# Performance work log

Measured on AMD Instinct MI355X. Metric: run time of the kernel, lower is better.

Reference implementation:

```python
import jax, jax.numpy as jnp
import numpy as np
from jax import lax

L = 2048        # leaves per tree
VOCAB = 50000
IN_DIM = 300
MEM = 150
HID = 50
NCLS = 5


def _balanced_tree(n_leaf):
    # children-before-parent topological order; node ids: [0, n_leaf) leaves,
    # [n_leaf, 2*n_leaf-1) internal, last id is the root's single child (ROOT is passthrough).
    level = list(range(n_leaf)); nid = n_leaf; lefts = []; rights = []
    while len(level) > 1:
        nxt = []
        for j in range(0, len(level) - 1, 2):
            lefts.append(level[j]); rights.append(level[j + 1]); nxt.append(nid); nid += 1
        if len(level) % 2:
            nxt.append(level[-1])
        level = nxt
    return np.asarray(lefts, np.int32), np.asarray(rights, np.int32)


def setup_inputs() -> dict:
    key = jax.random.key(0)
    ks = jax.random.split(key, 12)
    left, right = _balanced_tree(L)
    s = 0.05
    return {
        "l_tokens": jax.random.randint(ks[0], (L,), 0, VOCAB, dtype=jnp.int32),
        "r_tokens": jax.random.randint(ks[1], (L,), 0, VOCAB, dtype=jnp.int32),
        "left_idx": jnp.asarray(left),
        "right_idx": jnp.asarray(right),
        "emb": jax.random.normal(ks[2], (VOCAB, IN_DIM), jnp.float32) * s,
        "W_ioux": jax.random.normal(ks[3], (IN_DIM, 3 * MEM), jnp.float32) * s,
        "b_ioux": jnp.zeros((3 * MEM,), jnp.float32),
        "W_iouh": jax.random.normal(ks[4], (MEM, 3 * MEM), jnp.float32) * s,
        "b_iouh": jnp.zeros((3 * MEM,), jnp.float32),
        "W_fx": jax.random.normal(ks[5], (IN_DIM, MEM), jnp.float32) * s,
        "b_fx": jnp.zeros((MEM,), jnp.float32),
        "W_fh": jax.random.normal(ks[6], (MEM, MEM), jnp.float32) * s,
        "b_fh": jnp.zeros((MEM,), jnp.float32),
        "W_attn": jax.random.normal(ks[7], (2 * MEM, MEM), jnp.float32) * s,
        "b_attn": jnp.zeros((MEM,), jnp.float32),
        "W_wh": jax.random.normal(ks[8], (2 * MEM, HID), jnp.float32) * s,
        "b_wh": jnp.zeros((HID,), jnp.float32),
        "W_wp": jax.random.normal(ks[9], (HID, NCLS), jnp.float32) * s,
        "b_wp": jnp.zeros((NCLS,), jnp.float32),
    }


def _gates(iou):
    i, o, u = jnp.split(iou, 3, axis=-1)
    return jax.nn.sigmoid(i), jax.nn.sigmoid(o), jnp.tanh(u)


def _tree_lstm(tokens, left, right, emb, W_ioux, b_ioux, W_iouh, b_iouh, W_fh, b_fh):
    # Leaves (child_c = child_h = 0): iou = ioux(x) + iouh(0); fc term vanishes.
    x = emb[tokens]                                   # [L, in_dim]
    i, o, u = _gates(x @ W_ioux + b_ioux + b_iouh)
    c_leaf = i * u
    h_leaf = o * jnp.tanh(c_leaf)
    n_leaf = tokens.shape[0]
    N = 2 * n_leaf - 1
    C = jnp.zeros((N, MEM), x.dtype).at[:n_leaf].set(c_leaf)
    H = jnp.zeros((N, MEM), x.dtype).at[:n_leaf].set(h_leaf)

    # Internal nodes (inputs=None branch): iou = iouh(sum h_child); f_k = sigmoid(fh(h_k)).
    def step(carry, inp):
        C, H = carry
        k, li, ri = inp
        hl, hr = H[li], H[ri]
        i, o, u = _gates((hl + hr) @ W_iouh + b_iouh)
        fl = jax.nn.sigmoid(hl @ W_fh + b_fh)
        fr = jax.nn.sigmoid(hr @ W_fh + b_fh)
        c = i * u + fl * C[li] + fr * C[ri]
        h = o * jnp.tanh(c)
        return (C.at[k].set(c), H.at[k].set(h)), None

    ids = jnp.arange(n_leaf, N, dtype=jnp.int32)
    (C, H), _ = lax.scan(step, (C, H), (ids, left, right))
    return H  # [N, MEM]; H[-1] is the root hidden state (ROOT is passthrough)


def reference(l_tokens, r_tokens, left_idx, right_idx, emb, W_ioux, b_ioux, W_iouh, b_iouh, W_fx, b_fx, W_fh, b_fh, W_attn, b_attn, W_wh, b_wh, W_wp, b_wp):
    Hl = _tree_lstm(l_tokens, left_idx, right_idx, emb, W_ioux, b_ioux, W_iouh, b_iouh, W_fh, b_fh)
    Hr = _tree_lstm(r_tokens, left_idx, right_idx, emb, W_ioux, b_ioux, W_iouh, b_iouh, W_fh, b_fh)
    # Soft cross-attention over all node hidden states (torch code builds [Nr,Nl,m] beta;
    # here expressed as matmuls -- identical math).
    scores = Hl @ Hr.T                               # [Nl, Nr]
    beta_sum = jax.nn.softmax(scores, axis=1) @ Hr    # [Nl, MEM]
    alpha_sum = jax.nn.softmax(scores.T, axis=1) @ Hl  # [Nr, MEM]
    v_l = jnp.concatenate([Hl, beta_sum], axis=1) @ W_attn + b_attn
    v_r = jnp.concatenate([Hr, alpha_sum], axis=1) @ W_attn + b_attn
    lh = v_l[-1:]  # root hidden (root_idx is the root's matched row)
    rh = v_r[-1:]
    feats = jnp.concatenate([lh * rh, jnp.abs(lh - rh)], axis=1)
    hid = jax.nn.sigmoid(feats @ W_wh + b_wh)
    return jax.nn.log_softmax(hid @ W_wp + b_wp, axis=-1)  # [1, NCLS]
```

## Files before the change

kernel.cpp:

```cpp
#include <hip/hip_runtime.h>
#include <math.h>

#define LEAVES 2048
#define NN     4095
#define MEMD   150
#define IOUD   450
#define IND    300
#define STR    152
#define CT     4096


__device__ __forceinline__ float sigf(float x) { return 1.f / (1.f + expf(-x)); }

__global__ __launch_bounds__(256) void k_pack(
    const float* __restrict__ Wx, const float* __restrict__ Wh,
    const float* __restrict__ Wf,
    float4* __restrict__ PWx, float4* __restrict__ PWhf)
{
    int i = blockIdx.x * 256 + threadIdx.x;
    if (i < 45000) {
        int k = i / 150, d = i - k * 150;
        float4 v;
        v.x = Wx[k * IOUD + d];
        v.y = Wx[k * IOUD + 150 + d];
        v.z = Wx[k * IOUD + 300 + d];
        v.w = 0.f;
        PWx[i] = v;
    } else if (i < 67500) {
        int j = i - 45000;
        int k = j / 150, d = j - k * 150;
        float4 v;
        v.x = Wh[k * IOUD + d];
        v.y = Wh[k * IOUD + 150 + d];
        v.z = Wh[k * IOUD + 300 + d];
        v.w = Wf[k * MEMD + d];
        PWhf[j] = v;
    }
}

__global__ __launch_bounds__(640) void k_leaf(
    const int* __restrict__ ltok, const int* __restrict__ rtok,
    const float* __restrict__ emb, const float4* __restrict__ PWx,
    const float* __restrict__ bx, const float* __restrict__ bh,
    float* __restrict__ C, float* __restrict__ H)
{
    __shared__ float xs[IND][8];
    __shared__ int   tok[8];
    __shared__ float pb[300][13];
    const int tree = blockIdx.y, t = threadIdx.x;
    const int leaf0 = blockIdx.x << 3;
    const int* toks = tree ? rtok : ltok;

    if (t < 8) tok[t] = toks[leaf0 + t];
    __syncthreads();
    if (t < 600) {
        int q = t >> 3, m = t & 7;
        float4 v = *(const float4*)(emb + (size_t)tok[m] * IND + 4 * q);
        xs[4*q+0][m] = v.x; xs[4*q+1][m] = v.y;
        xs[4*q+2][m] = v.z; xs[4*q+3][m] = v.w;
    }
    __syncthreads();

    const int kh = (t >= 320) ? 1 : 0;
    const int tt = t - 320 * kh;
    const bool act = (tt < 300);
    const int hf = (tt >= 150) ? 1 : 0;
    const int d  = tt - 150 * hf;
    const int m0 = hf * 4;

    float ai[4], ao[4], au[4];
    if (act) {
        if (kh == 0) {
            const float bi = bx[d]       + bh[d];
            const float bo = bx[d + 150] + bh[d + 150];
            const float bu = bx[d + 300] + bh[d + 300];
            #pragma unroll
            for (int m = 0; m < 4; ++m) { ai[m] = bi; ao[m] = bo; au[m] = bu; }
        } else {
            #pragma unroll
            for (int m = 0; m < 4; ++m) { ai[m] = 0.f; ao[m] = 0.f; au[m] = 0.f; }
        }
        const float4* wp = PWx + d;
        const int kb = kh * 150;
        #pragma unroll 5
        for (int kk = 0; kk < 150; ++kk) {
            const int k = kb + kk;
            float4 w = wp[(size_t)k * 150];
            float4 x4 = *(const float4*)(&xs[k][m0]);
            float xv[4] = {x4.x, x4.y, x4.z, x4.w};
            #pragma unroll
            for (int m = 0; m < 4; ++m) {
                ai[m] = fmaf(xv[m], w.x, ai[m]);
                ao[m] = fmaf(xv[m], w.y, ao[m]);
                au[m] = fmaf(xv[m], w.z, au[m]);
            }
        }
    }
    if (kh == 1 && act) {
        #pragma unroll
        for (int m = 0; m < 4; ++m) {
            pb[tt][3*m + 0] = ai[m];
            pb[tt][3*m + 1] = ao[m];
            pb[tt][3*m + 2] = au[m];
        }
    }
    __syncthreads();
    if (kh == 0 && act) {
        float* Ct = C + ((size_t)tree * CT + leaf0 + m0) * STR;
        float* Ht = H + ((size_t)tree * CT + leaf0 + m0) * STR;
        #pragma unroll
        for (int m = 0; m < 4; ++m) {
            float aiv = ai[m] + pb[tt][3*m + 0];
            float aov = ao[m] + pb[tt][3*m + 1];
            float auv = au[m] + pb[tt][3*m + 2];
            float c = sigf(aiv) * tanhf(auv);
            float h = sigf(aov) * tanhf(c);
            Ct[(size_t)m * STR + d] = c;
            Ht[(size_t)m * STR + d] = h;
        }
    }
}

__global__ __launch_bounds__(640) void k_lvl(
    const float4* __restrict__ PWhf, const float* __restrict__ bh,
    const float* __restrict__ bf,
    float* __restrict__ C, float* __restrict__ H, int PB, int CB)
{
    __shared__ float buf[MEMD][8];
    __shared__ float pb[300][11];
    const int tree = blockIdx.y, t = threadIdx.x;
    const int p0 = blockIdx.x * 4;
    float* Ct = C + (size_t)tree * CT * STR;
    float* Ht = H + (size_t)tree * CT * STR;

    if (t < 600) {
        int m = t / 150, d2 = t - m * 150;
        int cc = CB + 2 * (p0 + m);
        float a = Ht[(size_t)cc * STR + d2];
        float b = Ht[(size_t)(cc + 1) * STR + d2];
        buf[d2][2*m + 0] = a + b;
        buf[d2][2*m + 1] = a;
    }
    __syncthreads();

    const int kh = (t >= 320) ? 1 : 0;
    const int tt = t - 320 * kh;
    const bool act = (tt < 300);
    const int hf = (tt >= 150) ? 1 : 0;
    const int d  = tt - 150 * hf;
    const int m0 = hf * 2;

    float ai[2], ao[2], au[2], afs[2], afl[2], cl[2], cr[2];
    if (act) {
        if (kh == 0) {
            const float bi = bh[d], bo = bh[d + 150], bu = bh[d + 300], bfv = bf[d];
            #pragma unroll
            for (int m = 0; m < 2; ++m) {
                ai[m] = bi; ao[m] = bo; au[m] = bu;
                afs[m] = 2.f * bfv; afl[m] = bfv;
                int cc = CB + 2 * (p0 + m0 + m);
                cl[m] = Ct[(size_t)cc * STR + d];
                cr[m] = Ct[(size_t)(cc + 1) * STR + d];
            }
        } else {
            #pragma unroll
            for (int m = 0; m < 2; ++m) {
                ai[m] = 0.f; ao[m] = 0.f; au[m] = 0.f; afs[m] = 0.f; afl[m] = 0.f;
            }
        }
        const float4* wp = PWhf + d;
        const int kb = kh * 75;
        #pragma unroll 5
        for (int kk = 0; kk < 75; ++kk) {
            const int k = kb + kk;
            float4 w = wp[(size_t)k * 150];
            float4 p4 = *(const float4*)(&buf[k][2 * m0]);
            float hs0 = p4.x, hl0 = p4.y, hs1 = p4.z, hl1 = p4.w;
            ai[0]  = fmaf(hs0, w.x, ai[0]);   ai[1]  = fmaf(hs1, w.x, ai[1]);
            ao[0]  = fmaf(hs0, w.y, ao[0]);   ao[1]  = fmaf(hs1, w.y, ao[1]);
            au[0]  = fmaf(hs0, w.z, au[0]);   au[1]  = fmaf(hs1, w.z, au[1]);
            afs[0] = fmaf(hs0, w.w, afs[0]);  afs[1] = fmaf(hs1, w.w, afs[1]);
            afl[0] = fmaf(hl0, w.w, afl[0]);  afl[1] = fmaf(hl1, w.w, afl[1]);
        }
    }
    if (kh == 1 && act) {
        #pragma unroll
        for (int m = 0; m < 2; ++m) {
            pb[tt][5*m + 0] = ai[m];
            pb[tt][5*m + 1] = ao[m];
            pb[tt][5*m + 2] = au[m];
            pb[tt][5*m + 3] = afs[m];
            pb[tt][5*m + 4] = afl[m];
        }
    }
    __syncthreads();
    if (kh == 0 && act) {
        #pragma unroll
        for (int m = 0; m < 2; ++m) {
            float aiv  = ai[m]  + pb[tt][5*m + 0];
            float aov  = ao[m]  + pb[tt][5*m + 1];
            float auv  = au[m]  + pb[tt][5*m + 2];
            float afsv = afs[m] + pb[tt][5*m + 3];
            float aflv = afl[m] + pb[tt][5*m + 4];
            float frv = afsv - aflv;
            float c = sigf(aiv) * tanhf(auv) + sigf(aflv) * cl[m] + sigf(frv) * cr[m];
            float h = sigf(aov) * tanhf(c);
            size_t rw = (size_t)(PB + p0 + m0 + m) * STR + d;
            Ct[rw] = c;
            Ht[rw] = h;
        }
    }
}

__global__ __launch_bounds__(640) void k_node(
    const float4* __restrict__ PWhf, const float* __restrict__ bh,
    const float* __restrict__ bf,
    float* __restrict__ C, float* __restrict__ H, int PB, int CB)
{
    __shared__ float hsv[MEMD], hlv[MEMD];
    __shared__ float part[4][5][152];
    const int tree = blockIdx.y, node = blockIdx.x, t = threadIdx.x;
    float* Ct = C + (size_t)tree * CT * STR;
    float* Ht = H + (size_t)tree * CT * STR;
    const int c0 = CB + 2 * node;

    if (t < MEMD) {
        float a = Ht[(size_t)c0 * STR + t];
        float b = Ht[(size_t)(c0 + 1) * STR + t];
        hsv[t] = a + b;
        hlv[t] = a;
    }
    __syncthreads();

    const int grp = t / 160, d = t - grp * 160;
    if (d < MEMD) {
        const int k0 = (grp * MEMD) >> 2;
        const int k1 = ((grp + 1) * MEMD) >> 2;
        float ai = 0.f, ao = 0.f, au = 0.f, afs = 0.f, afl = 0.f;
        const float4* wp = PWhf + d;
        #pragma unroll 4
        for (int k = k0; k < k1; ++k) {
            float4 w = wp[(size_t)k * 150];
            float hs = hsv[k], hl = hlv[k];
            ai  = fmaf(hs, w.x, ai);
            ao  = fmaf(hs, w.y, ao);
            au  = fmaf(hs, w.z, au);
            afs = fmaf(hs, w.w, afs);
            afl = fmaf(hl, w.w, afl);
        }
        part[grp][0][d] = ai;  part[grp][1][d] = ao;  part[grp][2][d] = au;
        part[grp][3][d] = afs; part[grp][4][d] = afl;
    }
    __syncthreads();

    if (t < MEMD) {
        const int d2 = t;
        float ai = bh[d2], ao = bh[d2 + 150], au = bh[d2 + 300];
        float bfv = bf[d2];
        float afs = 2.f * bfv, afl = bfv;
        #pragma unroll
        for (int g = 0; g < 4; ++g) {
            ai  += part[g][0][d2]; ao  += part[g][1][d2]; au += part[g][2][d2];
            afs += part[g][3][d2]; afl += part[g][4][d2];
        }
        float cl = Ct[(size_t)c0 * STR + d2];
        float cr = Ct[(size_t)(c0 + 1) * STR + d2];
        float frv = afs - afl;
        float c = sigf(ai) * tanhf(au) + sigf(afl) * cl + sigf(frv) * cr;
        float h = sigf(ao) * tanhf(c);
        size_t rw = (size_t)(PB + node) * STR + d2;
        Ct[rw] = c;
        Ht[rw] = h;
    }
}

__global__ __launch_bounds__(256) void k_attn(
    const float* __restrict__ H, float* __restrict__ cstat, float* __restrict__ part)
{
    __shared__ float lv[MEMD];
    __shared__ float sc[64];
    __shared__ float pv[64];
    const int bid = blockIdx.x, t = threadIdx.x;
    const int side = bid >> 6, chunk = bid & 63;
    const int j0 = chunk << 6;
    const int jn = min(64, NN - j0);
    const float* lastrow = H + ((size_t)side * CT + (NN - 1)) * STR;
    if (t < MEMD) lv[t] = lastrow[t];
    __syncthreads();

    const float* src = H + (size_t)(side ^ 1) * CT * STR + (size_t)j0 * STR;
    const int wave = t >> 6, lane = t & 63;
    for (int r = wave; r < jn; r += 4) {
        const float* row = src + (size_t)r * STR;
        float a = lv[lane] * row[lane] + lv[lane + 64] * row[lane + 64];
        if (lane < 22) a += lv[lane + 128] * row[lane + 128];
        #pragma unroll
        for (int off = 32; off; off >>= 1) a += __shfl_xor(a, off);
        if (lane == 0) sc[r] = a;
    }
    __syncthreads();
    if (wave == 0) {
        float v = (lane < jn) ? sc[lane] : -3.4e38f;
        float m = v;
        #pragma unroll
        for (int off = 32; off; off >>= 1) m = fmaxf(m, __shfl_xor(m, off));
        float e = (lane < jn) ? expf(v - m) : 0.f;
        pv[lane] = e;
        float s = e;
        #pragma unroll
        for (int off = 32; off; off >>= 1) s += __shfl_xor(s, off);
        if (lane == 0) {
            cstat[(side * 64 + chunk) * 2 + 0] = m;
            cstat[(side * 64 + chunk) * 2 + 1] = s;
        }
    }
    __syncthreads();
    if (t < MEMD) {
        float a = 0.f;
        for (int j = 0; j < jn; ++j) a += pv[j] * src[(size_t)j * STR + t];
        part[(size_t)(side * 64 + chunk) * STR + t] = a;
    }
}

__global__ __launch_bounds__(512) void k_final(
    const float* __restrict__ H, const float* __restrict__ cstat,
    const float* __restrict__ part,
    const float* __restrict__ Wattn, const float* __restrict__ battn,
    const float* __restrict__ Wwh, const float* __restrict__ bwh,
    const float* __restrict__ Wwp, const float* __restrict__ bwp,
    float* __restrict__ outp)
{
    __shared__ float scl[2][64];
    __shared__ float gseS[2];
    __shared__ float ba[300], catl[300], catr[300], vl[150], vr[150];
    __shared__ float feats[300], hid[50], logits[5];
    const int t = threadIdx.x, wave = t >> 6, lane = t & 63;

    if (wave < 2) {
        float lm = cstat[(wave * 64 + lane) * 2 + 0];
        float ls = cstat[(wave * 64 + lane) * 2 + 1];
        float m = lm;
        #pragma unroll
        for (int off = 32; off; off >>= 1) m = fmaxf(m, __shfl_xor(m, off));
        float s = expf(lm - m);
        scl[wave][lane] = s;
        float se = ls * s;
        #pragma unroll
        for (int off = 32; off; off >>= 1) se += __shfl_xor(se, off);
        if (lane == 0) gseS[wave] = se;
    }
    __syncthreads();
    if (t < 300) {
        int side = t / MEMD, d = t - side * MEMD;
        float a = 0.f;
        for (int c = 0; c < 64; ++c)
            a += part[(size_t)(side * 64 + c) * STR + d] * scl[side][c];
        ba[t] = a / gseS[side];
    }
    __syncthreads();
    const float* Hl_last = H + (size_t)(0 * CT + NN - 1) * STR;
    const float* Hr_last = H + (size_t)(1 * CT + NN - 1) * STR;
    if (t < MEMD) {
        catl[t] = Hl_last[t]; catl[150 + t] = ba[t];
        catr[t] = Hr_last[t]; catr[150 + t] = ba[150 + t];
    }
    __syncthreads();
    if (t < 300) {
        int d = (t < 150) ? t : t - 150;
        const float* cat = (t < 150) ? catl : catr;
        float a = battn[d];
        for (int k = 0; k < 300; ++k) a = fmaf(cat[k], Wattn[k * 150 + d], a);
        if (t < 150) vl[d] = a; else vr[d] = a;
    }
    __syncthreads();
    if (t < MEMD) {
        feats[t] = vl[t] * vr[t];
        feats[150 + t] = fabsf(vl[t] - vr[t]);
    }
    __syncthreads();
    if (t < 50) {
        float a = bwh[t];
        for (int k = 0; k < 300; ++k) a = fmaf(feats[k], Wwh[k * 50 + t], a);
        hid[t] = sigf(a);
    }
    __syncthreads();
    if (t < 5) {
        float a = bwp[t];
        for (int g = 0; g < 50; ++g) a = fmaf(hid[g], Wwp[g * 5 + t], a);
        logits[t] = a;
    }
    __syncthreads();
    if (t == 0) {
        float m = logits[0];
        for (int c = 1; c < 5; ++c) m = fmaxf(m, logits[c]);
        float s = 0.f;
        for (int c = 0; c < 5; ++c) s += expf(logits[c] - m);
        float lse = m + logf(s);
        for (int c = 0; c < 5; ++c) outp[c] = logits[c] - lse;
    }
}

extern "C" void kernel_launch(void* const* d_in, const int* in_sizes, int n_in,
                              void* d_out, int out_size, void* d_ws, size_t ws_size,
                              hipStream_t stream)
{
    const int*   ltok  = (const int*)d_in[0];
    const int*   rtok  = (const int*)d_in[1];
    const float* emb   = (const float*)d_in[4];
    const float* Wx    = (const float*)d_in[5];
    const float* bx    = (const float*)d_in[6];
    const float* Wh    = (const float*)d_in[7];
    const float* bh    = (const float*)d_in[8];
    const float* Wf    = (const float*)d_in[11];
    const float* bf    = (const float*)d_in[12];
    const float* Wattn = (const float*)d_in[13];
    const float* battn = (const float*)d_in[14];
    const float* Wwh   = (const float*)d_in[15];
    const float* bwh   = (const float*)d_in[16];
    const float* Wwp   = (const float*)d_in[17];
    const float* bwp   = (const float*)d_in[18];
    float* out = (float*)d_out;

    float* ws    = (float*)d_ws;
    float*  C    = ws;
    float*  H    = C + (size_t)2 * CT * STR;
    float*  cs   = H + (size_t)2 * CT * STR;
    float*  part = cs + 256;
    float4* PWx  = (float4*)(part + (size_t)128 * STR);
    float4* PWhf = PWx + 45000;

    k_pack<<<dim3(264), dim3(256), 0, stream>>>(Wx, Wh, Wf, PWx, PWhf);

    k_leaf<<<dim3(256, 2), dim3(640), 0, stream>>>(ltok, rtok, emb, PWx, bx, bh, C, H);

    k_lvl<<<dim3(256, 2), dim3(640), 0, stream>>>(PWhf, bh, bf, C, H, 2048, 0);
    k_lvl<<<dim3(128, 2), dim3(640), 0, stream>>>(PWhf, bh, bf, C, H, 3072, 2048);
    k_lvl<<<dim3(64,  2), dim3(640), 0, stream>>>(PWhf, bh, bf, C, H, 3584, 3072);

    k_node<<<dim3(128, 2), dim3(640), 0, stream>>>(PWhf, bh, bf, C, H, 3840, 3584);
    k_node<<<dim3(64,  2), dim3(640), 0, stream>>>(PWhf, bh, bf, C, H, 3968, 3840);
    k_node<<<dim3(32,  2), dim3(640), 0, stream>>>(PWhf, bh, bf, C, H, 4032, 3968);
    k_node<<<dim3(16,  2), dim3(640), 0, stream>>>(PWhf, bh, bf, C, H, 4064, 4032);
    k_node<<<dim3(8,   2), dim3(640), 0, stream>>>(PWhf, bh, bf, C, H, 4080, 4064);
    k_node<<<dim3(4,   2), dim3(640), 0, stream>>>(PWhf, bh, bf, C, H, 4088, 4080);
    k_node<<<dim3(2,   2), dim3(640), 0, stream>>>(PWhf, bh, bf, C, H, 4092, 4088);
    k_node<<<dim3(1,   2), dim3(640), 0, stream>>>(PWhf, bh, bf, C, H, 4094, 4092);

    k_attn<<<dim3(128), dim3(256), 0, stream>>>(H, cs, part);
    k_final<<<dim3(1), dim3(512), 0, stream>>>(H, cs, part, Wattn, battn,
                                               Wwh, bwh, Wwp, bwp, out);
}
```

Baseline: 150.5 us.

## Drop Wx packing and restructure leaf kernel to 4 leaves per block

Removes the packing of W_ioux into interleaved float4 form, so the leaf kernel reads the original weight layout directly with three coalesced scalar loads per k. The leaf kernel now handles 4 leaves per 320-thread block instead of 8 per 640 threads. Each wave splits the K reduction across its two 32-lane halves and combines them with a cross-lane shuffle instead of a shared-memory partial buffer and an extra barrier. This shrinks the pack kernel and cuts LDS and sync work, but each weight element is now fetched by twice as many blocks.

Result: slower. 155.3 us (+3.2%).

```diff
diff --git a/kernel.cpp b/kernel.cpp
--- a/kernel.cpp
+++ b/kernel.cpp
@@ -13,108 +13,87 @@
 __device__ __forceinline__ float sigf(float x) { return 1.f / (1.f + expf(-x)); }
 
 __global__ __launch_bounds__(256) void k_pack(
-    const float* __restrict__ Wx, const float* __restrict__ Wh,
-    const float* __restrict__ Wf,
-    float4* __restrict__ PWx, float4* __restrict__ PWhf)
+    const float* __restrict__ Wh, const float* __restrict__ Wf,
+    float4* __restrict__ PWhf)
 {
     int i = blockIdx.x * 256 + threadIdx.x;
-    if (i < 45000) {
+    if (i < 22500) {
         int k = i / 150, d = i - k * 150;
-        float4 v;
-        v.x = Wx[k * IOUD + d];
-        v.y = Wx[k * IOUD + 150 + d];
-        v.z = Wx[k * IOUD + 300 + d];
-        v.w = 0.f;
-        PWx[i] = v;
-    } else if (i < 67500) {
-        int j = i - 45000;
-        int k = j / 150, d = j - k * 150;
         float4 v;
         v.x = Wh[k * IOUD + d];
         v.y = Wh[k * IOUD + 150 + d];
         v.z = Wh[k * IOUD + 300 + d];
         v.w = Wf[k * MEMD + d];
-        PWhf[j] = v;
-    }
-}
-
-__global__ __launch_bounds__(640) void k_leaf(
+        PWhf[i] = v;
+    }
+}
+
+__global__ __launch_bounds__(320) void k_leaf(
     const int* __restrict__ ltok, const int* __restrict__ rtok,
-    const float* __restrict__ emb, const float4* __restrict__ PWx,
+    const float* __restrict__ emb, const float* __restrict__ Wx,
     const float* __restrict__ bx, const float* __restrict__ bh,
     float* __restrict__ C, float* __restrict__ H)
 {
-    __shared__ float xs[IND][8];
-    __shared__ int   tok[8];
-    __shared__ float pb[300][13];
+    __shared__ __align__(16) float xs[IND][4];
+    __shared__ int tok[4];
     const int tree = blockIdx.y, t = threadIdx.x;
-    const int leaf0 = blockIdx.x << 3;
+    const int leaf0 = blockIdx.x << 2;
     const int* toks = tree ? rtok : ltok;
 
-    if (t < 8) tok[t] = toks[leaf0 + t];
-    __syncthreads();
-    if (t < 600) {
-        int q = t >> 3, m = t & 7;
+    if (t < 4) tok[t] = toks[leaf0 + t];
+    __syncthreads();
+    if (t < 300) {
+        int q = t >> 2, m = t & 3;
         float4 v = *(const float4*)(emb + (size_t)tok[m] * IND + 4 * q);
         xs[4*q+0][m] = v.x; xs[4*q+1][m] = v.y;
         xs[4*q+2][m] = v.z; xs[4*q+3][m] = v.w;
     }
     __syncthreads();
 
-    const int kh = (t >= 320) ? 1 : 0;
-    const int tt = t - 320 * kh;
-    const bool act = (tt < 300);
-    const int hf = (tt >= 150) ? 1 : 0;
-    const int d  = tt - 150 * hf;
-    const int m0 = hf * 4;
-
-    float ai[4], ao[4], au[4];
-    if (act) {
-        if (kh == 0) {
-            const float bi = bx[d]       + bh[d];
-            const float bo = bx[d + 150] + bh[d + 150];
-            const float bu = bx[d + 300] + bh[d + 300];
-            #pragma unroll
-            for (int m = 0; m < 4; ++m) { ai[m] = bi; ao[m] = bo; au[m] = bu; }
-        } else {
-            #pragma unroll
-            for (int m = 0; m < 4; ++m) { ai[m] = 0.f; ao[m] = 0.f; au[m] = 0.f; }
-        }
-        const float4* wp = PWx + d;
-        const int kb = kh * 150;
-        #pragma unroll 5
-        for (int kk = 0; kk < 150; ++kk) {
-            const int k = kb + kk;
-            float4 w = wp[(size_t)k * 150];
-            float4 x4 = *(const float4*)(&xs[k][m0]);
-            float xv[4] = {x4.x, x4.y, x4.z, x4.w};
-            #pragma unroll
-            for (int m = 0; m < 4; ++m) {
-                ai[m] = fmaf(xv[m], w.x, ai[m]);
-                ao[m] = fmaf(xv[m], w.y, ao[m]);
-                au[m] = fmaf(xv[m], w.z, au[m]);
-            }
-        }
-    }
-    if (kh == 1 && act) {
+    const int lane = t & 63, w = t >> 6;
+    const int kh = lane >> 5;
+    const int d  = w * 32 + (lane & 31);
+    const bool act = (d < 150);
+
+    float ai[4] = {0.f,0.f,0.f,0.f};
+    float ao[4] = {0.f,0.f,0.f,0.f};
+    float au[4] = {0.f,0.f,0.f,0.f};
+
+    const float* wp = Wx + (act ? d : 0);
+    const int kb = kh * 150;
+    #pragma unroll 5
+    for (int kk = 0; kk < 150; ++kk) {
+        const int k = kb + kk;
+        float wi = wp[k * IOUD];
+        float wo = wp[k * IOUD + 150];
+        float wu = wp[k * IOUD + 300];
+        float4 x4 = *(const float4*)(&xs[k][0]);
+        float xv[4] = {x4.x, x4.y, x4.z, x4.w};
         #pragma unroll
         for (int m = 0; m < 4; ++m) {
-            pb[tt][3*m + 0] = ai[m];
-            pb[tt][3*m + 1] = ao[m];
-            pb[tt][3*m + 2] = au[m];
-        }
-    }
-    __syncthreads();
-    if (kh == 0 && act) {
-        float* Ct = C + ((size_t)tree * CT + leaf0 + m0) * STR;
-        float* Ht = H + ((size_t)tree * CT + leaf0 + m0) * STR;
+            ai[m] = fmaf(xv[m], wi, ai[m]);
+            ao[m] = fmaf(xv[m], wo, ao[m]);
+            au[m] = fmaf(xv[m], wu, au[m]);
+        }
+    }
+
+    #pragma unroll
+    for (int m = 0; m < 4; ++m) {
+        ai[m] += __shfl_xor(ai[m], 32);
+        ao[m] += __shfl_xor(ao[m], 32);
+        au[m] += __shfl_xor(au[m], 32);
+    }
+
+    if (act && kh == 0) {
+        const float bi = bx[d]       + bh[d];
+        const float bo = bx[d + 150] + bh[d + 150];
+        const float bu = bx[d + 300] + bh[d + 300];
+        float* Ct = C + ((size_t)tree * CT + leaf0) * STR;
+        float* Ht = H + ((size_t)tree * CT + leaf0) * STR;
         #pragma unroll
         for (int m = 0; m < 4; ++m) {
-            float aiv = ai[m] + pb[tt][3*m + 0];
-            float aov = ao[m] + pb[tt][3*m + 1];
-            float auv = au[m] + pb[tt][3*m + 2];
-            float c = sigf(aiv) * tanhf(auv);
-            float h = sigf(aov) * tanhf(c);
+            float c = sigf(ai[m] + bi) * tanhf(au[m] + bu);
+            float h = sigf(ao[m] + bo) * tanhf(c);
             Ct[(size_t)m * STR + d] = c;
             Ht[(size_t)m * STR + d] = h;
         }
@@ -426,12 +405,11 @@
     float*  H    = C + (size_t)2 * CT * STR;
     float*  cs   = H + (size_t)2 * CT * STR;
     float*  part = cs + 256;
-    float4* PWx  = (float4*)(part + (size_t)128 * STR);
-    float4* PWhf = PWx + 45000;
-
-    k_pack<<<dim3(264), dim3(256), 0, stream>>>(Wx, Wh, Wf, PWx, PWhf);
-
-    k_leaf<<<dim3(256, 2), dim3(640), 0, stream>>>(ltok, rtok, emb, PWx, bx, bh, C, H);
+    float4* PWhf = (float4*)(part + (size_t)128 * STR);
+
+    k_pack<<<dim3(88), dim3(256), 0, stream>>>(Wh, Wf, PWhf);
+
+    k_leaf<<<dim3(512, 2), dim3(320), 0, stream>>>(ltok, rtok, emb, Wx, bx, bh, C, H);
 
     k_lvl<<<dim3(256, 2), dim3(640), 0, stream>>>(PWhf, bh, bf, C, H, 2048, 0);
     k_lvl<<<dim3(128, 2), dim3(640), 0, stream>>>(PWhf, bh, bf, C, H, 3072, 2048);
```
